# Kernel tuning notes

Hardware: AMD Instinct MI355X
Metric: run time of the kernel (lower is better)

The kernel has to match this reference:

```python
import jax, jax.numpy as jnp
import numpy as np


def setup_inputs() -> dict:
    key = jax.random.key(0)
    # [batch, 2 (real/imag), proj_nums, det_nums]
    x = jax.random.normal(key, (16, 2, 1024, 1024), dtype=jnp.float32)
    return {"x": x}


def reference(x) -> jnp.ndarray:
    # Split stacked real/imag channels -> complex frequency-domain sinogram.
    re, im = jnp.split(x, 2, axis=1)          # each [B, 1, P, D]
    c = (re + 1j * im).astype(jnp.complex64)
    # Batched row-wise inverse FFT along detector axis (replaces the
    # per-(batch, row) Python loop of cuFFT calls in the original).
    y = jnp.real(jnp.fft.ifft(jnp.fft.ifftshift(c, axes=-1), axis=-1))
    # Global min-max normalization over the whole tensor.
    y_min = jnp.min(y)
    y_max = jnp.max(y)
    return (y - y_min) / (y_max - y_min)
```

## Files before the change

kernel.cpp:

```cpp
#include <hip/hip_runtime.h>

#define FFT_N 1024
#define NPART 4096

__device__ __forceinline__ int br6(int x) { return (int)(__brev((unsigned)x) >> 26); }

__device__ __forceinline__ unsigned int f2key(float f) {
    unsigned int u = __float_as_uint(f);
    return (u & 0x80000000u) ? ~u : (u | 0x80000000u);
}
__device__ __forceinline__ float key2f(unsigned int k) {
    unsigned int u = (k & 0x80000000u) ? (k & 0x7FFFFFFFu) : ~k;
    return __uint_as_float(u);
}

__global__ void init_mm(unsigned int* mm) {
    mm[0] = 0xFFFFFFFFu;
    mm[1] = 0u;
}

template <bool USE_ATOMIC>
__global__ __launch_bounds__(256) void ifft_rows(const float* __restrict__ x,
                                                 float* __restrict__ out,
                                                 float* __restrict__ partials,
                                                 unsigned int* __restrict__ mm) {
    const int t    = threadIdx.x;
    const int lane = t & 63;
    const int wid  = t >> 6;
    const int row  = blockIdx.x * 4 + wid;
    const int b    = row >> 10;
    const int p    = row & 1023;
    const float* re = x + (((size_t)(b * 2) * 1024) + p) * 1024;
    const float* im = re + (size_t)1024 * 1024;

    float ar[16], ai[16];
    #pragma unroll
    for (int q = 0; q < 4; ++q) {
        float4 v = *reinterpret_cast<const float4*>(re + 16 * lane + 4 * q);
        ar[4 * q] = v.x; ar[4 * q + 1] = v.y; ar[4 * q + 2] = v.z; ar[4 * q + 3] = v.w;
    }
    #pragma unroll
    for (int q = 0; q < 4; ++q) {
        float4 w = *reinterpret_cast<const float4*>(im + 16 * lane + 4 * q);
        ai[4 * q] = w.x; ai[4 * q + 1] = w.y; ai[4 * q + 2] = w.z; ai[4 * q + 3] = w.w;
    }

    #pragma unroll
    for (int st = 0; st < 6; ++st) {
        const int h  = 32 >> st;
        const bool hi = (lane & h) != 0;
        const float s = hi ? -1.0f : 1.0f;
        if (h > 1) {
            const int j = lane & (h - 1);
            float ang = hi ? (3.14159265358979323846f / (float)h) * (float)j : 0.0f;
            float ws, wc;
            __sincosf(ang, &ws, &wc);
            #pragma unroll
            for (int r = 0; r < 16; ++r) {
                float pr = __shfl_xor(ar[r], h);
                float pi = __shfl_xor(ai[r], h);
                float tr = fmaf(s, ar[r], pr);
                float ti = fmaf(s, ai[r], pi);
                ar[r] = tr * wc - ti * ws;
                ai[r] = tr * ws + ti * wc;
            }
        } else {
            #pragma unroll
            for (int r = 0; r < 16; ++r) {
                float pr = __shfl_xor(ar[r], 1);
                float pi = __shfl_xor(ai[r], 1);
                ar[r] = fmaf(s, ar[r], pr);
                ai[r] = fmaf(s, ai[r], pi);
            }
        }
    }

    const int k1 = br6(lane);
    const float theta = 6.283185307179586f * (float)k1 * (1.0f / 1024.0f);
    #pragma unroll
    for (int r = 1; r < 16; ++r) {
        float sn, cs;
        __sincosf(theta * (float)r, &sn, &cs);
        float vr = ar[r], vi = ai[r];
        ar[r] = vr * cs - vi * sn;
        ai[r] = vr * sn + vi * cs;
    }

    float yr[16], yi[16];
    #pragma unroll
    for (int a = 0; a < 4; ++a) {
        float t0r = ar[a] + ar[a + 8],      t0i = ai[a] + ai[a + 8];
        float t1r = ar[a] - ar[a + 8],      t1i = ai[a] - ai[a + 8];
        float t2r = ar[a + 4] + ar[a + 12], t2i = ai[a + 4] + ai[a + 12];
        float t3r = ar[a + 4] - ar[a + 12], t3i = ai[a + 4] - ai[a + 12];
        yr[a]      = t0r + t2r;  yi[a]      = t0i + t2i;
        yr[a + 4]  = t1r - t3i;  yi[a + 4]  = t1i + t3r;
        yr[a + 8]  = t0r - t2r;  yi[a + 8]  = t0i - t2i;
        yr[a + 12] = t1r + t3i;  yi[a + 12] = t1i - t3r;
    }
    constexpr float W16R_[10] = { 1.0f, 0.92387953251f, 0.70710678119f, 0.38268343236f,
                                  0.0f, 0.0f, -0.70710678119f, 0.0f, 0.0f, -0.92387953251f };
    constexpr float W16I_[10] = { 0.0f, 0.38268343236f, 0.70710678119f, 0.92387953251f,
                                  1.0f, 0.0f, 0.70710678119f, 0.0f, 0.0f, -0.38268343236f };
    float vals[16];
    const float scale = (lane & 32) ? -9.765625e-4f : 9.765625e-4f;
    #pragma unroll
    for (int c = 0; c < 4; ++c) {
        float zr0 = yr[4 * c];
        float zr1, zi1, zr2, zr3, zi3;
        { float wr = W16R_[c],     wi = W16I_[c];
          float vr = yr[1 + 4 * c], vi = yi[1 + 4 * c];
          zr1 = vr * wr - vi * wi; zi1 = vr * wi + vi * wr; }
        { float wr = W16R_[2 * c], wi = W16I_[2 * c];
          float vr = yr[2 + 4 * c], vi = yi[2 + 4 * c];
          zr2 = vr * wr - vi * wi; }
        { float wr = W16R_[3 * c], wi = W16I_[3 * c];
          float vr = yr[3 + 4 * c], vi = yi[3 + 4 * c];
          zr3 = vr * wr - vi * wi; zi3 = vr * wi + vi * wr; }
        float u0r = zr0 + zr2, u1r = zr0 - zr2;
        float u2r = zr1 + zr3;
        float u3i = zi1 - zi3;
        vals[c]      = (u0r + u2r) * scale;
        vals[c + 4]  = (u1r - u3i) * scale;
        vals[c + 8]  = (u0r - u2r) * scale;
        vals[c + 12] = (u1r + u3i) * scale;
    }

    float vmin = INFINITY, vmax = -INFINITY;
    #pragma unroll
    for (int k2 = 0; k2 < 16; ++k2) {
        vmin = fminf(vmin, vals[k2]);
        vmax = fmaxf(vmax, vals[k2]);
    }
    float* orow = out + (size_t)row * FFT_N;
    #pragma unroll
    for (int k2 = 0; k2 < 16; ++k2) {
        orow[k1 + (k2 << 6)] = vals[k2];
    }

    #pragma unroll
    for (int off = 32; off >= 1; off >>= 1) {
        vmin = fminf(vmin, __shfl_xor(vmin, off));
        vmax = fmaxf(vmax, __shfl_xor(vmax, off));
    }
    __shared__ float smn[4], smx[4];
    if ((t & 63) == 0) { smn[wid] = vmin; smx[wid] = vmax; }
    __syncthreads();
    if (t == 0) {
        float mn = fminf(fminf(smn[0], smn[1]), fminf(smn[2], smn[3]));
        float mx = fmaxf(fmaxf(smx[0], smx[1]), fmaxf(smx[2], smx[3]));
        if (USE_ATOMIC) {
            atomicMin(&mm[0], f2key(mn));
            atomicMax(&mm[1], f2key(mx));
        } else {
            partials[2 * blockIdx.x]     = mn;
            partials[2 * blockIdx.x + 1] = mx;
        }
    }
}

__global__ __launch_bounds__(256) void reduce_mm(const float* __restrict__ partials,
                                                 float* __restrict__ mm) {
    float mn = INFINITY, mx = -INFINITY;
    for (int i = threadIdx.x; i < NPART; i += 256) {
        float2 v = reinterpret_cast<const float2*>(partials)[i];
        mn = fminf(mn, v.x);
        mx = fmaxf(mx, v.y);
    }
    #pragma unroll
    for (int off = 32; off >= 1; off >>= 1) {
        mn = fminf(mn, __shfl_xor(mn, off));
        mx = fmaxf(mx, __shfl_xor(mx, off));
    }
    __shared__ float smn[4], smx[4];
    const int wid = threadIdx.x >> 6;
    if ((threadIdx.x & 63) == 0) { smn[wid] = mn; smx[wid] = mx; }
    __syncthreads();
    if (threadIdx.x == 0) {
        mm[0] = fminf(fminf(smn[0], smn[1]), fminf(smn[2], smn[3]));
        mm[1] = fmaxf(fmaxf(smx[0], smx[1]), fmaxf(smx[2], smx[3]));
    }
}

template <bool FROM_KEYS>
__global__ __launch_bounds__(256) void normalize_k(float* __restrict__ out,
                                                   const void* __restrict__ mmv,
                                                   int n4) {
    float mn, mx;
    if (FROM_KEYS) {
        const unsigned int* mm = (const unsigned int*)mmv;
        mn = key2f(mm[0]); mx = key2f(mm[1]);
    } else {
        const float* mm = (const float*)mmv;
        mn = mm[0]; mx = mm[1];
    }
    const float inv = 1.0f / (mx - mn);
    float4* o4 = reinterpret_cast<float4*>(out);
    for (int i = blockIdx.x * blockDim.x + threadIdx.x; i < n4;
         i += gridDim.x * blockDim.x) {
        float4 v = o4[i];
        v.x = (v.x - mn) * inv;
        v.y = (v.y - mn) * inv;
        v.z = (v.z - mn) * inv;
        v.w = (v.w - mn) * inv;
        o4[i] = v;
    }
}

extern "C" void kernel_launch(void* const* d_in, const int* in_sizes, int n_in,
                              void* d_out, int out_size, void* d_ws, size_t ws_size,
                              hipStream_t stream) {
    const float* x = (const float*)d_in[0];
    float* out = (float*)d_out;
    const int n4 = out_size / 4;

    if (ws_size >= (size_t)(2 * NPART + 2) * sizeof(float)) {
        float* partials = (float*)d_ws;
        float* mm = partials + 2 * NPART;
        hipLaunchKernelGGL((ifft_rows<false>), dim3(NPART), dim3(256), 0, stream,
                           x, out, partials, nullptr);
        hipLaunchKernelGGL(reduce_mm, dim3(1), dim3(256), 0, stream, partials, mm);
        hipLaunchKernelGGL((normalize_k<false>), dim3(2048), dim3(256), 0, stream,
                           out, (const void*)mm, n4);
    } else {
        unsigned int* mm = (unsigned int*)d_ws;
        hipLaunchKernelGGL(init_mm, dim3(1), dim3(1), 0, stream, mm);
        hipLaunchKernelGGL((ifft_rows<true>), dim3(NPART), dim3(256), 0, stream,
                           x, out, nullptr, mm);
        hipLaunchKernelGGL((normalize_k<true>), dim3(2048), dim3(256), 0, stream,
                           out, (const void*)mm, n4);
    }
}
```

Baseline: 72.69 us.

## Recompute the row IFFT in a second pass instead of re-reading the unnormalized output

The pipeline becomes two passes over the input. The first computes the row IFFTs and only the global min/max via atomics, and the second recomputes the IFFTs and writes normalized values directly with nontemporal stores. This removes the write of the unnormalized output plus the separate read-modify-write normalize pass, at the cost of reading the input twice and doing the FFT arithmetic twice. The partials/reduce path is dropped in favour of atomics. Input is 128MB and output 64MB, so traffic goes from roughly 128+64+128 to 256+64 MB.

```diff
diff --git a/kernel.cpp b/kernel.cpp
--- a/kernel.cpp
+++ b/kernel.cpp
@@ -1,7 +1,7 @@
 #include <hip/hip_runtime.h>
 
 #define FFT_N 1024
-#define NPART 4096
+#define GRID_ROWS 4096
 
 __device__ __forceinline__ int br6(int x) { return (int)(__brev((unsigned)x) >> 26); }
 
@@ -19,17 +19,10 @@
     mm[1] = 0u;
 }
 
-template <bool USE_ATOMIC>
-__global__ __launch_bounds__(256) void ifft_rows(const float* __restrict__ x,
-                                                 float* __restrict__ out,
-                                                 float* __restrict__ partials,
-                                                 unsigned int* __restrict__ mm) {
-    const int t    = threadIdx.x;
-    const int lane = t & 63;
-    const int wid  = t >> 6;
-    const int row  = blockIdx.x * 4 + wid;
-    const int b    = row >> 10;
-    const int p    = row & 1023;
+__device__ __forceinline__ void fft_row_vals(const float* __restrict__ x,
+                                             int row, int lane, float* vals) {
+    const int b = row >> 10;
+    const int p = row & 1023;
     const float* re = x + (((size_t)(b * 2) * 1024) + p) * 1024;
     const float* im = re + (size_t)1024 * 1024;
 
@@ -102,7 +95,6 @@
                                   0.0f, 0.0f, -0.70710678119f, 0.0f, 0.0f, -0.92387953251f };
     constexpr float W16I_[10] = { 0.0f, 0.38268343236f, 0.70710678119f, 0.92387953251f,
                                   1.0f, 0.0f, 0.70710678119f, 0.0f, 0.0f, -0.38268343236f };
-    float vals[16];
     const float scale = (lane & 32) ? -9.765625e-4f : 9.765625e-4f;
     #pragma unroll
     for (int c = 0; c < 4; ++c) {
@@ -125,6 +117,17 @@
         vals[c + 8]  = (u0r - u2r) * scale;
         vals[c + 12] = (u1r + u3i) * scale;
     }
+}
+
+__global__ __launch_bounds__(256) void minmax_pass(const float* __restrict__ x,
+                                                   unsigned int* __restrict__ mm) {
+    const int t    = threadIdx.x;
+    const int lane = t & 63;
+    const int wid  = t >> 6;
+    const int row  = blockIdx.x * 4 + wid;
+
+    float vals[16];
+    fft_row_vals(x, row, lane, vals);
 
     float vmin = INFINITY, vmax = -INFINITY;
     #pragma unroll
@@ -132,12 +135,6 @@
         vmin = fminf(vmin, vals[k2]);
         vmax = fmaxf(vmax, vals[k2]);
     }
-    float* orow = out + (size_t)row * FFT_N;
-    #pragma unroll
-    for (int k2 = 0; k2 < 16; ++k2) {
-        orow[k1 + (k2 << 6)] = vals[k2];
-    }
-
     #pragma unroll
     for (int off = 32; off >= 1; off >>= 1) {
         vmin = fminf(vmin, __shfl_xor(vmin, off));
@@ -149,61 +146,30 @@
     if (t == 0) {
         float mn = fminf(fminf(smn[0], smn[1]), fminf(smn[2], smn[3]));
         float mx = fmaxf(fmaxf(smx[0], smx[1]), fmaxf(smx[2], smx[3]));
-        if (USE_ATOMIC) {
-            atomicMin(&mm[0], f2key(mn));
-            atomicMax(&mm[1], f2key(mx));
-        } else {
-            partials[2 * blockIdx.x]     = mn;
-            partials[2 * blockIdx.x + 1] = mx;
-        }
+        atomicMin(&mm[0], f2key(mn));
+        atomicMax(&mm[1], f2key(mx));
     }
 }
 
-__global__ __launch_bounds__(256) void reduce_mm(const float* __restrict__ partials,
-                                                 float* __restrict__ mm) {
-    float mn = INFINITY, mx = -INFINITY;
-    for (int i = threadIdx.x; i < NPART; i += 256) {
-        float2 v = reinterpret_cast<const float2*>(partials)[i];
-        mn = fminf(mn, v.x);
-        mx = fmaxf(mx, v.y);
-    }
+__global__ __launch_bounds__(256) void write_pass(const float* __restrict__ x,
+                                                  float* __restrict__ out,
+                                                  const unsigned int* __restrict__ mm) {
+    const int t    = threadIdx.x;
+    const int lane = t & 63;
+    const int wid  = t >> 6;
+    const int row  = blockIdx.x * 4 + wid;
+
+    const float mn  = key2f(mm[0]);
+    const float inv = 1.0f / (key2f(mm[1]) - mn);
+
+    float vals[16];
+    fft_row_vals(x, row, lane, vals);
+
+    const int k1 = br6(lane);
+    float* orow = out + (size_t)row * FFT_N;
     #pragma unroll
-    for (int off = 32; off >= 1; off >>= 1) {
-        mn = fminf(mn, __shfl_xor(mn, off));
-        mx = fmaxf(mx, __shfl_xor(mx, off));
-    }
-    __shared__ float smn[4], smx[4];
-    const int wid = threadIdx.x >> 6;
-    if ((threadIdx.x & 63) == 0) { smn[wid] = mn; smx[wid] = mx; }
-    __syncthreads();
-    if (threadIdx.x == 0) {
-        mm[0] = fminf(fminf(smn[0], smn[1]), fminf(smn[2], smn[3]));
-        mm[1] = fmaxf(fmaxf(smx[0], smx[1]), fmaxf(smx[2], smx[3]));
-    }
-}
-
-template <bool FROM_KEYS>
-__global__ __launch_bounds__(256) void normalize_k(float* __restrict__ out,
-                                                   const void* __restrict__ mmv,
-                                                   int n4) {
-    float mn, mx;
-    if (FROM_KEYS) {
-        const unsigned int* mm = (const unsigned int*)mmv;
-        mn = key2f(mm[0]); mx = key2f(mm[1]);
-    } else {
-        const float* mm = (const float*)mmv;
-        mn = mm[0]; mx = mm[1];
-    }
-    const float inv = 1.0f / (mx - mn);
-    float4* o4 = reinterpret_cast<float4*>(out);
-    for (int i = blockIdx.x * blockDim.x + threadIdx.x; i < n4;
-         i += gridDim.x * blockDim.x) {
-        float4 v = o4[i];
-        v.x = (v.x - mn) * inv;
-        v.y = (v.y - mn) * inv;
-        v.z = (v.z - mn) * inv;
-        v.w = (v.w - mn) * inv;
-        o4[i] = v;
+    for (int k2 = 0; k2 < 16; ++k2) {
+        __builtin_nontemporal_store((vals[k2] - mn) * inv, orow + k1 + (k2 << 6));
     }
 }
 
@@ -212,22 +178,9 @@
                               hipStream_t stream) {
     const float* x = (const float*)d_in[0];
     float* out = (float*)d_out;
-    const int n4 = out_size / 4;
+    unsigned int* mm = (unsigned int*)d_ws;
 
-    if (ws_size >= (size_t)(2 * NPART + 2) * sizeof(float)) {
-        float* partials = (float*)d_ws;
-        float* mm = partials + 2 * NPART;
-        hipLaunchKernelGGL((ifft_rows<false>), dim3(NPART), dim3(256), 0, stream,
-                           x, out, partials, nullptr);
-        hipLaunchKernelGGL(reduce_mm, dim3(1), dim3(256), 0, stream, partials, mm);
-        hipLaunchKernelGGL((normalize_k<false>), dim3(2048), dim3(256), 0, stream,
-                           out, (const void*)mm, n4);
-    } else {
-        unsigned int* mm = (unsigned int*)d_ws;
-        hipLaunchKernelGGL(init_mm, dim3(1), dim3(1), 0, stream, mm);
-        hipLaunchKernelGGL((ifft_rows<true>), dim3(NPART), dim3(256), 0, stream,
-                           x, out, nullptr, mm);
-        hipLaunchKernelGGL((normalize_k<true>), dim3(2048), dim3(256), 0, stream,
-                           out, (const void*)mm, n4);
-    }
+    hipLaunchKernelGGL(init_mm, dim3(1), dim3(1), 0, stream, mm);
+    hipLaunchKernelGGL(minmax_pass, dim3(GRID_ROWS), dim3(256), 0, stream, x, mm);
+    hipLaunchKernelGGL(write_pass, dim3(GRID_ROWS), dim3(256), 0, stream, x, out, mm);
 }
```

After: 150.9 us. 108% more time.

## Fuse IFFT, min-max reduction and normalization into one cooperative kernel

Applied to the files above, without the earlier changes.

Replaces the three-kernel sequence (IFFT with partial min/max, reduction, normalize pass) with a single cooperative launch of 1024 blocks. Each wave handles four rows and keeps their results on chip, two in shared memory and two in registers, across a grid-wide sync. After the sync it reads the global min/max and writes normalized output once with nontemporal stores. This removes the second full read and write of the 64MB output and two launch overheads. In exchange it raises register and LDS pressure (32KB LDS per block), needs 4 resident blocks per CU for cooperative residency, and pays the cost of a grid barrier.

```diff
diff --git a/kernel.cpp b/kernel.cpp
--- a/kernel.cpp
+++ b/kernel.cpp
@@ -1,7 +1,11 @@
 #include <hip/hip_runtime.h>
+#include <hip/hip_cooperative_groups.h>
+
+namespace cg = cooperative_groups;
 
 #define FFT_N 1024
 #define NPART 4096
+#define COOP_BLOCKS 1024
 
 __device__ __forceinline__ int br6(int x) { return (int)(__brev((unsigned)x) >> 26); }
 
@@ -19,17 +23,10 @@
     mm[1] = 0u;
 }
 
-template <bool USE_ATOMIC>
-__global__ __launch_bounds__(256) void ifft_rows(const float* __restrict__ x,
-                                                 float* __restrict__ out,
-                                                 float* __restrict__ partials,
-                                                 unsigned int* __restrict__ mm) {
-    const int t    = threadIdx.x;
-    const int lane = t & 63;
-    const int wid  = t >> 6;
-    const int row  = blockIdx.x * 4 + wid;
-    const int b    = row >> 10;
-    const int p    = row & 1023;
+__device__ __forceinline__ void fft_row_vals(const float* __restrict__ x,
+                                             int row, int lane, float* vals) {
+    const int b = row >> 10;
+    const int p = row & 1023;
     const float* re = x + (((size_t)(b * 2) * 1024) + p) * 1024;
     const float* im = re + (size_t)1024 * 1024;
 
@@ -102,7 +99,6 @@
                                   0.0f, 0.0f, -0.70710678119f, 0.0f, 0.0f, -0.92387953251f };
     constexpr float W16I_[10] = { 0.0f, 0.38268343236f, 0.70710678119f, 0.92387953251f,
                                   1.0f, 0.0f, 0.70710678119f, 0.0f, 0.0f, -0.38268343236f };
-    float vals[16];
     const float scale = (lane & 32) ? -9.765625e-4f : 9.765625e-4f;
     #pragma unroll
     for (int c = 0; c < 4; ++c) {
@@ -125,6 +121,126 @@
         vals[c + 8]  = (u0r - u2r) * scale;
         vals[c + 12] = (u1r + u3i) * scale;
     }
+}
+
+__global__ __launch_bounds__(256, 4) void fused_pass(const float* __restrict__ x,
+                                                     float* __restrict__ out,
+                                                     float* __restrict__ partials) {
+    cg::grid_group grid = cg::this_grid();
+    const int t    = threadIdx.x;
+    const int lane = t & 63;
+    const int w    = t >> 6;
+    const int bid  = blockIdx.x;
+    const int base_row = bid * 16 + w * 4;
+
+    __shared__ float lds[4][2][FFT_N];
+    __shared__ float smn[4], smx[4], bmm[2];
+
+    float vmin = INFINITY, vmax = -INFINITY;
+    float keep2[16], keep3[16];
+
+    {
+        float vals[16];
+        fft_row_vals(x, base_row + 0, lane, vals);
+        #pragma unroll
+        for (int k2 = 0; k2 < 16; ++k2) {
+            lds[w][0][k2 * 64 + lane] = vals[k2];
+            vmin = fminf(vmin, vals[k2]); vmax = fmaxf(vmax, vals[k2]);
+        }
+    }
+    {
+        float vals[16];
+        fft_row_vals(x, base_row + 1, lane, vals);
+        #pragma unroll
+        for (int k2 = 0; k2 < 16; ++k2) {
+            lds[w][1][k2 * 64 + lane] = vals[k2];
+            vmin = fminf(vmin, vals[k2]); vmax = fmaxf(vmax, vals[k2]);
+        }
+    }
+    fft_row_vals(x, base_row + 2, lane, keep2);
+    #pragma unroll
+    for (int k2 = 0; k2 < 16; ++k2) {
+        vmin = fminf(vmin, keep2[k2]); vmax = fmaxf(vmax, keep2[k2]);
+    }
+    fft_row_vals(x, base_row + 3, lane, keep3);
+    #pragma unroll
+    for (int k2 = 0; k2 < 16; ++k2) {
+        vmin = fminf(vmin, keep3[k2]); vmax = fmaxf(vmax, keep3[k2]);
+    }
+
+    #pragma unroll
+    for (int off = 32; off >= 1; off >>= 1) {
+        vmin = fminf(vmin, __shfl_xor(vmin, off));
+        vmax = fmaxf(vmax, __shfl_xor(vmax, off));
+    }
+    if ((t & 63) == 0) { smn[w] = vmin; smx[w] = vmax; }
+    __syncthreads();
+    if (t == 0) {
+        float mn = fminf(fminf(smn[0], smn[1]), fminf(smn[2], smn[3]));
+        float mx = fmaxf(fmaxf(smx[0], smx[1]), fmaxf(smx[2], smx[3]));
+        reinterpret_cast<float2*>(partials)[bid] = make_float2(mn, mx);
+    }
+
+    grid.sync();
+
+    float mn = INFINITY, mx = -INFINITY;
+    #pragma unroll
+    for (int it = 0; it < COOP_BLOCKS / 256; ++it) {
+        float2 v = reinterpret_cast<const float2*>(partials)[t + it * 256];
+        mn = fminf(mn, v.x); mx = fmaxf(mx, v.y);
+    }
+    #pragma unroll
+    for (int off = 32; off >= 1; off >>= 1) {
+        mn = fminf(mn, __shfl_xor(mn, off));
+        mx = fmaxf(mx, __shfl_xor(mx, off));
+    }
+    if ((t & 63) == 0) { smn[w] = mn; smx[w] = mx; }
+    __syncthreads();
+    if (t == 0) {
+        bmm[0] = fminf(fminf(smn[0], smn[1]), fminf(smn[2], smn[3]));
+        bmm[1] = fmaxf(fmaxf(smx[0], smx[1]), fmaxf(smx[2], smx[3]));
+    }
+    __syncthreads();
+
+    const float MN  = bmm[0];
+    const float INV = 1.0f / (bmm[1] - MN);
+    const int k1 = br6(lane);
+
+    {
+        float* orow = out + (size_t)(base_row + 2) * FFT_N;
+        #pragma unroll
+        for (int k2 = 0; k2 < 16; ++k2)
+            __builtin_nontemporal_store((keep2[k2] - MN) * INV, orow + k1 + (k2 << 6));
+    }
+    {
+        float* orow = out + (size_t)(base_row + 3) * FFT_N;
+        #pragma unroll
+        for (int k2 = 0; k2 < 16; ++k2)
+            __builtin_nontemporal_store((keep3[k2] - MN) * INV, orow + k1 + (k2 << 6));
+    }
+    #pragma unroll
+    for (int j = 0; j < 2; ++j) {
+        float* orow = out + (size_t)(base_row + j) * FFT_N;
+        #pragma unroll
+        for (int k2 = 0; k2 < 16; ++k2) {
+            float v = lds[w][j][k2 * 64 + lane];
+            __builtin_nontemporal_store((v - MN) * INV, orow + k1 + (k2 << 6));
+        }
+    }
+}
+
+template <bool USE_ATOMIC>
+__global__ __launch_bounds__(256) void ifft_rows(const float* __restrict__ x,
+                                                 float* __restrict__ out,
+                                                 float* __restrict__ partials,
+                                                 unsigned int* __restrict__ mm) {
+    const int t    = threadIdx.x;
+    const int lane = t & 63;
+    const int wid  = t >> 6;
+    const int row  = blockIdx.x * 4 + wid;
+
+    float vals[16];
+    fft_row_vals(x, row, lane, vals);
 
     float vmin = INFINITY, vmax = -INFINITY;
     #pragma unroll
@@ -132,11 +248,10 @@
         vmin = fminf(vmin, vals[k2]);
         vmax = fmaxf(vmax, vals[k2]);
     }
+    const int k1 = br6(lane);
     float* orow = out + (size_t)row * FFT_N;
     #pragma unroll
-    for (int k2 = 0; k2 < 16; ++k2) {
-        orow[k1 + (k2 << 6)] = vals[k2];
-    }
+    for (int k2 = 0; k2 < 16; ++k2) orow[k1 + (k2 << 6)] = vals[k2];
 
     #pragma unroll
     for (int off = 32; off >= 1; off >>= 1) {
@@ -213,6 +328,15 @@
     const float* x = (const float*)d_in[0];
     float* out = (float*)d_out;
     const int n4 = out_size / 4;
+
+    if (ws_size >= (size_t)(2 * COOP_BLOCKS) * sizeof(float)) {
+        float* partials = (float*)d_ws;
+        void* args[3] = { (void*)&x, (void*)&out, (void*)&partials };
+        hipError_t e = hipLaunchCooperativeKernel((const void*)fused_pass,
+                                                  dim3(COOP_BLOCKS), dim3(256),
+                                                  args, 0, stream);
+        if (e == hipSuccess) return;
+    }
 
     if (ws_size >= (size_t)(2 * NPART + 2) * sizeof(float)) {
         float* partials = (float*)d_ws;
```

Result: slower. 145.5 us (+100.2%).

## Compute real-output IFFT via half-length complex FFT with Hermitian packing

Applied to the files above, without the earlier changes.

Replaces the full 1024-point complex inverse FFT per row with a 512-point complex FFT. The even/odd real outputs are packed into one complex sequence by combining X[k], X[k+512], X[512-k] and X[-k] with a twiddle. This halves the butterfly and shuffle work and lets each lane write 16 contiguous outputs as float4 stores instead of strided scalar stores. In exchange, input loads become scalar with mirrored indices rather than float4 vectors, and launch bounds now request 4 blocks per SM.

```diff
diff --git a/kernel.cpp b/kernel.cpp
--- a/kernel.cpp
+++ b/kernel.cpp
@@ -1,7 +1,7 @@
 #include <hip/hip_runtime.h>
 
 #define FFT_N 1024
-#define NPART 4096
+#define NROWBLK 4096
 
 __device__ __forceinline__ int br6(int x) { return (int)(__brev((unsigned)x) >> 26); }
 
@@ -19,11 +19,104 @@
     mm[1] = 0u;
 }
 
+__device__ __forceinline__ void zifft_row(const float* __restrict__ re,
+                                          const float* __restrict__ im,
+                                          int lane, float* vals) {
+    float ur[8], ui[8], pr[8], pi[8], qr[8], qi[8], vr[8], vi[8];
+    #pragma unroll
+    for (int j = 0; j < 8; ++j) {
+        const int k  = lane + 64 * j;
+        const int iq = 512 - k;
+        const int iv = (1024 - k) & 1023;
+        ur[j] = re[k];       ui[j] = im[k];
+        pr[j] = re[k + 512]; pi[j] = im[k + 512];
+        qr[j] = re[iq];      qi[j] = im[iq];
+        vr[j] = re[iv];      vi[j] = im[iv];
+    }
+
+    float Zr[8], Zi[8];
+    #pragma unroll
+    for (int j = 0; j < 8; ++j) {
+        const int k = lane + 64 * j;
+        float Ar = pr[j] + ur[j] + qr[j] + vr[j];
+        float Ai = pi[j] + ui[j] - qi[j] - vi[j];
+        float Br = pr[j] - ur[j] + qr[j] - vr[j];
+        float Bi = pi[j] - ui[j] - qi[j] + vi[j];
+        float s, c;
+        __sincosf(6.283185307179586e-3f * 0.9765625f * (float)k, &s, &c);
+        Zr[j] = Ar - (c * Bi + s * Br);
+        Zi[j] = Ai + (c * Br - s * Bi);
+    }
+
+    const float R = 0.70710678118654752f;
+    float tr, ti;
+    tr = Zr[0]-Zr[4]; ti = Zi[0]-Zi[4]; Zr[0]+=Zr[4]; Zi[0]+=Zi[4]; Zr[4]=tr;        Zi[4]=ti;
+    tr = Zr[1]-Zr[5]; ti = Zi[1]-Zi[5]; Zr[1]+=Zr[5]; Zi[1]+=Zi[5]; Zr[5]=R*(tr-ti); Zi[5]=R*(tr+ti);
+    tr = Zr[2]-Zr[6]; ti = Zi[2]-Zi[6]; Zr[2]+=Zr[6]; Zi[2]+=Zi[6]; Zr[6]=-ti;       Zi[6]=tr;
+    tr = Zr[3]-Zr[7]; ti = Zi[3]-Zi[7]; Zr[3]+=Zr[7]; Zi[3]+=Zi[7]; Zr[7]=-R*(tr+ti);Zi[7]=R*(tr-ti);
+    tr = Zr[0]-Zr[2]; ti = Zi[0]-Zi[2]; Zr[0]+=Zr[2]; Zi[0]+=Zi[2]; Zr[2]=tr;  Zi[2]=ti;
+    tr = Zr[1]-Zr[3]; ti = Zi[1]-Zi[3]; Zr[1]+=Zr[3]; Zi[1]+=Zi[3]; Zr[3]=-ti; Zi[3]=tr;
+    tr = Zr[4]-Zr[6]; ti = Zi[4]-Zi[6]; Zr[4]+=Zr[6]; Zi[4]+=Zi[6]; Zr[6]=tr;  Zi[6]=ti;
+    tr = Zr[5]-Zr[7]; ti = Zi[5]-Zi[7]; Zr[5]+=Zr[7]; Zi[5]+=Zi[7]; Zr[7]=-ti; Zi[7]=tr;
+    tr = Zr[0]-Zr[1]; ti = Zi[0]-Zi[1]; Zr[0]+=Zr[1]; Zi[0]+=Zi[1]; Zr[1]=tr; Zi[1]=ti;
+    tr = Zr[2]-Zr[3]; ti = Zi[2]-Zi[3]; Zr[2]+=Zr[3]; Zi[2]+=Zi[3]; Zr[3]=tr; Zi[3]=ti;
+    tr = Zr[4]-Zr[5]; ti = Zi[4]-Zi[5]; Zr[4]+=Zr[5]; Zi[4]+=Zi[5]; Zr[5]=tr; Zi[5]=ti;
+    tr = Zr[6]-Zr[7]; ti = Zi[6]-Zi[7]; Zr[6]+=Zr[7]; Zi[6]+=Zi[7]; Zr[7]=tr; Zi[7]=ti;
+
+    constexpr int BR3[8] = {0, 4, 2, 6, 1, 5, 3, 7};
+    #pragma unroll
+    for (int t = 1; t < 8; ++t) {
+        float ang = 1.2271846303085129e-2f * (float)(lane * BR3[t]);
+        float s, c;
+        __sincosf(ang, &s, &c);
+        float xr = Zr[t], xi = Zi[t];
+        Zr[t] = xr * c - xi * s;
+        Zi[t] = xr * s + xi * c;
+    }
+
+    #pragma unroll
+    for (int st = 0; st < 6; ++st) {
+        const int h   = 32 >> st;
+        const bool hi = (lane & h) != 0;
+        const float sgn = hi ? -1.0f : 1.0f;
+        if (h > 1) {
+            const int j = lane & (h - 1);
+            float ang = hi ? (3.14159265358979323846f / (float)h) * (float)j : 0.0f;
+            float ws, wc;
+            __sincosf(ang, &ws, &wc);
+            #pragma unroll
+            for (int r = 0; r < 8; ++r) {
+                float prt = __shfl_xor(Zr[r], h);
+                float pit = __shfl_xor(Zi[r], h);
+                float t1 = fmaf(sgn, Zr[r], prt);
+                float t2 = fmaf(sgn, Zi[r], pit);
+                Zr[r] = t1 * wc - t2 * ws;
+                Zi[r] = t1 * ws + t2 * wc;
+            }
+        } else {
+            #pragma unroll
+            for (int r = 0; r < 8; ++r) {
+                float prt = __shfl_xor(Zr[r], 1);
+                float pit = __shfl_xor(Zi[r], 1);
+                Zr[r] = fmaf(sgn, Zr[r], prt);
+                Zi[r] = fmaf(sgn, Zi[r], pit);
+            }
+        }
+    }
+
+    const float SC = 4.8828125e-4f;
+    #pragma unroll
+    for (int t = 0; t < 8; ++t) {
+        vals[2 * BR3[t]]     = Zr[t] * SC;
+        vals[2 * BR3[t] + 1] = Zi[t] * SC;
+    }
+}
+
 template <bool USE_ATOMIC>
-__global__ __launch_bounds__(256) void ifft_rows(const float* __restrict__ x,
-                                                 float* __restrict__ out,
-                                                 float* __restrict__ partials,
-                                                 unsigned int* __restrict__ mm) {
+__global__ __launch_bounds__(256, 4) void zifft_rows(const float* __restrict__ x,
+                                                     float* __restrict__ out,
+                                                     float* __restrict__ partials,
+                                                     unsigned int* __restrict__ mm) {
     const int t    = threadIdx.x;
     const int lane = t & 63;
     const int wid  = t >> 6;
@@ -33,109 +126,21 @@
     const float* re = x + (((size_t)(b * 2) * 1024) + p) * 1024;
     const float* im = re + (size_t)1024 * 1024;
 
-    float ar[16], ai[16];
+    float vals[16];
+    zifft_row(re, im, lane, vals);
+
+    float vmin = INFINITY, vmax = -INFINITY;
+    #pragma unroll
+    for (int i = 0; i < 16; ++i) {
+        vmin = fminf(vmin, vals[i]);
+        vmax = fmaxf(vmax, vals[i]);
+    }
+
+    float* obase = out + (size_t)row * FFT_N + 16 * br6(lane);
     #pragma unroll
     for (int q = 0; q < 4; ++q) {
-        float4 v = *reinterpret_cast<const float4*>(re + 16 * lane + 4 * q);
-        ar[4 * q] = v.x; ar[4 * q + 1] = v.y; ar[4 * q + 2] = v.z; ar[4 * q + 3] = v.w;
-    }
-    #pragma unroll
-    for (int q = 0; q < 4; ++q) {
-        float4 w = *reinterpret_cast<const float4*>(im + 16 * lane + 4 * q);
-        ai[4 * q] = w.x; ai[4 * q + 1] = w.y; ai[4 * q + 2] = w.z; ai[4 * q + 3] = w.w;
-    }
-
-    #pragma unroll
-    for (int st = 0; st < 6; ++st) {
-        const int h  = 32 >> st;
-        const bool hi = (lane & h) != 0;
-        const float s = hi ? -1.0f : 1.0f;
-        if (h > 1) {
-            const int j = lane & (h - 1);
-            float ang = hi ? (3.14159265358979323846f / (float)h) * (float)j : 0.0f;
-            float ws, wc;
-            __sincosf(ang, &ws, &wc);
-            #pragma unroll
-            for (int r = 0; r < 16; ++r) {
-                float pr = __shfl_xor(ar[r], h);
-                float pi = __shfl_xor(ai[r], h);
-                float tr = fmaf(s, ar[r], pr);
-                float ti = fmaf(s, ai[r], pi);
-                ar[r] = tr * wc - ti * ws;
-                ai[r] = tr * ws + ti * wc;
-            }
-        } else {
-            #pragma unroll
-            for (int r = 0; r < 16; ++r) {
-                float pr = __shfl_xor(ar[r], 1);
-                float pi = __shfl_xor(ai[r], 1);
-                ar[r] = fmaf(s, ar[r], pr);
-                ai[r] = fmaf(s, ai[r], pi);
-            }
-        }
-    }
-
-    const int k1 = br6(lane);
-    const float theta = 6.283185307179586f * (float)k1 * (1.0f / 1024.0f);
-    #pragma unroll
-    for (int r = 1; r < 16; ++r) {
-        float sn, cs;
-        __sincosf(theta * (float)r, &sn, &cs);
-        float vr = ar[r], vi = ai[r];
-        ar[r] = vr * cs - vi * sn;
-        ai[r] = vr * sn + vi * cs;
-    }
-
-    float yr[16], yi[16];
-    #pragma unroll
-    for (int a = 0; a < 4; ++a) {
-        float t0r = ar[a] + ar[a + 8],      t0i = ai[a] + ai[a + 8];
-        float t1r = ar[a] - ar[a + 8],      t1i = ai[a] - ai[a + 8];
-        float t2r = ar[a + 4] + ar[a + 12], t2i = ai[a + 4] + ai[a + 12];
-        float t3r = ar[a + 4] - ar[a + 12], t3i = ai[a + 4] - ai[a + 12];
-        yr[a]      = t0r + t2r;  yi[a]      = t0i + t2i;
-        yr[a + 4]  = t1r - t3i;  yi[a + 4]  = t1i + t3r;
-        yr[a + 8]  = t0r - t2r;  yi[a + 8]  = t0i - t2i;
-        yr[a + 12] = t1r + t3i;  yi[a + 12] = t1i - t3r;
-    }
-    constexpr float W16R_[10] = { 1.0f, 0.92387953251f, 0.70710678119f, 0.38268343236f,
-                                  0.0f, 0.0f, -0.70710678119f, 0.0f, 0.0f, -0.92387953251f };
-    constexpr float W16I_[10] = { 0.0f, 0.38268343236f, 0.70710678119f, 0.92387953251f,
-                                  1.0f, 0.0f, 0.70710678119f, 0.0f, 0.0f, -0.38268343236f };
-    float vals[16];
-    const float scale = (lane & 32) ? -9.765625e-4f : 9.765625e-4f;
-    #pragma unroll
-    for (int c = 0; c < 4; ++c) {
-        float zr0 = yr[4 * c];
-        float zr1, zi1, zr2, zr3, zi3;
-        { float wr = W16R_[c],     wi = W16I_[c];
-          float vr = yr[1 + 4 * c], vi = yi[1 + 4 * c];
-          zr1 = vr * wr - vi * wi; zi1 = vr * wi + vi * wr; }
-        { float wr = W16R_[2 * c], wi = W16I_[2 * c];
-          float vr = yr[2 + 4 * c], vi = yi[2 + 4 * c];
-          zr2 = vr * wr - vi * wi; }
-        { float wr = W16R_[3 * c], wi = W16I_[3 * c];
-          float vr = yr[3 + 4 * c], vi = yi[3 + 4 * c];
-          zr3 = vr * wr - vi * wi; zi3 = vr * wi + vi * wr; }
-        float u0r = zr0 + zr2, u1r = zr0 - zr2;
-        float u2r = zr1 + zr3;
-        float u3i = zi1 - zi3;
-        vals[c]      = (u0r + u2r) * scale;
-        vals[c + 4]  = (u1r - u3i) * scale;
-        vals[c + 8]  = (u0r - u2r) * scale;
-        vals[c + 12] = (u1r + u3i) * scale;
-    }
-
-    float vmin = INFINITY, vmax = -INFINITY;
-    #pragma unroll
-    for (int k2 = 0; k2 < 16; ++k2) {
-        vmin = fminf(vmin, vals[k2]);
-        vmax = fmaxf(vmax, vals[k2]);
-    }
-    float* orow = out + (size_t)row * FFT_N;
-    #pragma unroll
-    for (int k2 = 0; k2 < 16; ++k2) {
-        orow[k1 + (k2 << 6)] = vals[k2];
+        *reinterpret_cast<float4*>(obase + 4 * q) =
+            make_float4(vals[4 * q], vals[4 * q + 1], vals[4 * q + 2], vals[4 * q + 3]);
     }
 
     #pragma unroll
@@ -162,7 +167,7 @@
 __global__ __launch_bounds__(256) void reduce_mm(const float* __restrict__ partials,
                                                  float* __restrict__ mm) {
     float mn = INFINITY, mx = -INFINITY;
-    for (int i = threadIdx.x; i < NPART; i += 256) {
+    for (int i = threadIdx.x; i < NROWBLK; i += 256) {
         float2 v = reinterpret_cast<const float2*>(partials)[i];
         mn = fminf(mn, v.x);
         mx = fmaxf(mx, v.y);
@@ -214,10 +219,10 @@
     float* out = (float*)d_out;
     const int n4 = out_size / 4;
 
-    if (ws_size >= (size_t)(2 * NPART + 2) * sizeof(float)) {
+    if (ws_size >= (size_t)(2 * NROWBLK + 2) * sizeof(float)) {
         float* partials = (float*)d_ws;
-        float* mm = partials + 2 * NPART;
-        hipLaunchKernelGGL((ifft_rows<false>), dim3(NPART), dim3(256), 0, stream,
+        float* mm = partials + 2 * NROWBLK;
+        hipLaunchKernelGGL((zifft_rows<false>), dim3(NROWBLK), dim3(256), 0, stream,
                            x, out, partials, nullptr);
         hipLaunchKernelGGL(reduce_mm, dim3(1), dim3(256), 0, stream, partials, mm);
         hipLaunchKernelGGL((normalize_k<false>), dim3(2048), dim3(256), 0, stream,
@@ -225,7 +230,7 @@
     } else {
         unsigned int* mm = (unsigned int*)d_ws;
         hipLaunchKernelGGL(init_mm, dim3(1), dim3(1), 0, stream, mm);
-        hipLaunchKernelGGL((ifft_rows<true>), dim3(NPART), dim3(256), 0, stream,
+        hipLaunchKernelGGL((zifft_rows<true>), dim3(NROWBLK), dim3(256), 0, stream,
                            x, out, nullptr, mm);
         hipLaunchKernelGGL((normalize_k<true>), dim3(2048), dim3(256), 0, stream,
                            out, (const void*)mm, n4);
```

Result: faster. 67.93 us (-6.5%).
